# Optimization experiments

Measured on AMD Instinct MI355X. Metric: run time of the kernel, lower is better.

Reference implementation:

```python
import jax, jax.numpy as jnp
import numpy as np

UNITS = 256
IN_DIM = 256
OUT_DIM = 10
TOL = 1e-4
MAX_ITER = 50


def setup_inputs() -> dict:
    key = jax.random.key(0)
    ks = jax.random.split(key, 16)
    B = 65536
    s = 1.0 / np.sqrt(UNITS)
    inp = {
        "x": jax.random.normal(ks[0], (B, IN_DIM), dtype=jnp.float32),
        "w_in": jax.random.normal(ks[1], (IN_DIM, UNITS), dtype=jnp.float32) * s,
        "b_in": jax.random.normal(ks[2], (UNITS,), dtype=jnp.float32) * 0.01,
        "w_out": jax.random.normal(ks[3], (UNITS, OUT_DIM), dtype=jnp.float32) * s,
        "b_out": jax.random.normal(ks[4], (OUT_DIM,), dtype=jnp.float32) * 0.01,
    }
    eye = jnp.eye(UNITS, dtype=jnp.float32)
    for i in range(4):
        # well-conditioned (invertible) implicit-layer weight: I + small perturbation
        inp[f"w{i+1}"] = eye + 0.1 * jax.random.normal(ks[5 + 2 * i], (UNITS, UNITS), dtype=jnp.float32) * s
        inp[f"b{i+1}"] = jax.random.normal(ks[6 + 2 * i], (UNITS,), dtype=jnp.float32) * 0.01
    return inp


def newton_block(x, W, b):
    # Solve z @ W = x + tanh(x) + b by Newton iteration with early exit on ||g||.
    c = x + jnp.tanh(x) + b  # [B, n]
    z0 = x
    g0 = z0 @ W - c

    def cond(state):
        z, g, it = state
        return (it < MAX_ITER) & (jnp.linalg.norm(g) >= TOL)

    def body(state):
        z, g, it = state
        # torch.solve(g[:, :, None], W^T.repeat(B,1,1)): shared matrix -> one solve
        z = z - jnp.linalg.solve(W.T, g.T).T
        g = z @ W - c
        return (z, g, it + 1)

    z, _, _ = jax.lax.while_loop(cond, body, (z0, g0, jnp.asarray(0)))
    z = jax.lax.stop_gradient(z)  # torch loop runs under no_grad
    # final differentiable correction (torch: z = z - (z@W - x - tanh(x) - b))
    return z - (z @ W - c)


def reference(x, w_in, b_in, w1, b1, w2, b2, w3, b3, w4, b4, w_out, b_out):
    z = x @ w_in + b_in
    z = newton_block(z, w1, b1)
    z = newton_block(z, w2, b2)
    z = newton_block(z, w3, b3)
    z = newton_block(z, w4, b4)
    logits = z @ w_out + b_out
    return jax.nn.softmax(logits, axis=1)
```

## Files before the change

### kernel.cpp

```cpp
#include <hip/hip_runtime.h>
#include <hip/hip_fp16.h>
#include <math.h>


typedef __attribute__((ext_vector_type(8))) short short8;
typedef __attribute__((ext_vector_type(4))) float f32x4;

__device__ __forceinline__ float tanh_fast(float x) {
#if __has_builtin(__builtin_amdgcn_exp2f)
  float e = __builtin_amdgcn_exp2f(x * 2.8853900817779268f);
#else
  float e = __expf(2.0f * x);
#endif
  return 1.0f - 2.0f * __builtin_amdgcn_rcpf(e + 1.0f);
}
__device__ __forceinline__ unsigned rn_pair16(float v0, float v1) {
  __half2 h = __floats2half2_rn(v0, v1);
  return *reinterpret_cast<unsigned*>(&h);
}

__global__ __launch_bounds__(256) void ns_gemm_k(
    const float* __restrict__ a0, const float* __restrict__ a1,
    const float* __restrict__ a2, const float* __restrict__ a3,
    const float* __restrict__ b0, const float* __restrict__ b1,
    const float* __restrict__ b2, const float* __restrict__ b3,
    float* __restrict__ D, float bDiag, int eMode,
    const float* __restrict__ w_in, const float* __restrict__ w_out,
    unsigned* __restrict__ pk) {
  int m = blockIdx.z;
  int t = threadIdx.x;
  if (m == 4) {
    int base = (blockIdx.y * 8 + blockIdx.x) * 256 + t;
    for (int idx = base; idx < 34816; idx += 16384) {
      if (idx < 32768) {
        int kc = idx >> 12;
        int nt = (idx >> 8) & 15;
        int lane = (idx >> 2) & 63;
        int d = idx & 3;
        int n = nt * 16 + (lane & 15);
        int kb = kc * 32 + (lane >> 4) * 8 + d * 2;
        pk[idx] = rn_pair16(w_in[kb * 256 + n], w_in[(kb + 1) * 256 + n]);
      } else {
        int r2 = idx - 32768;
        int kc = r2 >> 8;
        int lane = (r2 >> 2) & 63;
        int d = r2 & 3;
        int n = lane & 15;
        int kb = kc * 32 + (lane >> 4) * 8 + d * 2;
        float v0 = (n < 10) ? w_out[kb * 10 + n] : 0.0f;
        float v1 = (n < 10) ? w_out[(kb + 1) * 10 + n] : 0.0f;
        pk[5 * 32768 + r2] = rn_pair16(v0, v1);
      }
    }
    return;
  }
  __shared__ float As[32][17];
  __shared__ float Bs[16][33];
  const float* A = (m == 0) ? a0 : (m == 1) ? a1 : (m == 2) ? a2 : a3;
  const float* B = (m == 0) ? b0 : (m == 1) ? b1 : (m == 2) ? b2 : b3;
  float* Dm = D + m * 65536;
  int tx = t & 15, ty = t >> 4;
  int row0 = blockIdx.y * 32, col0 = blockIdx.x * 32;
  float acc00 = 0.f, acc01 = 0.f, acc10 = 0.f, acc11 = 0.f;
  for (int k0 = 0; k0 < 256; k0 += 16) {
#pragma unroll
    for (int half = 0; half < 2; ++half) {
      int e = t + half * 256;
      int r = e >> 4, kk = e & 15;
      As[r][kk] = A[(row0 + r) * 256 + k0 + kk];
      int k2 = e >> 5, c = e & 31;
      float w = B[(k0 + k2) * 256 + col0 + c];
      if (bDiag != 0.0f) w = (((k0 + k2) == (col0 + c)) ? bDiag : 0.0f) - w;
      Bs[k2][c] = w;
    }
    __syncthreads();
#pragma unroll
    for (int kk = 0; kk < 16; ++kk) {
      float av0 = As[ty][kk], av1 = As[ty + 16][kk];
      float bv0 = Bs[kk][tx], bv1 = Bs[kk][tx + 16];
      acc00 = fmaf(av0, bv0, acc00);
      acc01 = fmaf(av0, bv1, acc01);
      acc10 = fmaf(av1, bv0, acc10);
      acc11 = fmaf(av1, bv1, acc11);
    }
    __syncthreads();
  }
  if (eMode) {
    acc00 = (((row0 + ty) == (col0 + tx)) ? 3.f : 0.f) - acc00;
    acc01 = (((row0 + ty) == (col0 + tx + 16)) ? 3.f : 0.f) - acc01;
    acc10 = (((row0 + ty + 16) == (col0 + tx)) ? 3.f : 0.f) - acc10;
    acc11 = (((row0 + ty + 16) == (col0 + tx + 16)) ? 3.f : 0.f) - acc11;
  }
  Dm[(row0 + ty) * 256 + col0 + tx] = acc00;
  Dm[(row0 + ty) * 256 + col0 + tx + 16] = acc01;
  Dm[(row0 + ty + 16) * 256 + col0 + tx] = acc10;
  Dm[(row0 + ty + 16) * 256 + col0 + tx + 16] = acc11;
}

__global__ __launch_bounds__(256) void ns_pack_k(
    const float* __restrict__ w1a, const float* __restrict__ w2a,
    const float* __restrict__ w3a, const float* __restrict__ w4a,
    const float* __restrict__ V, unsigned* __restrict__ pk) {
  __shared__ float As[32][17];
  __shared__ float Bs[16][33];
  __shared__ float Dt[32][33];
  int m = blockIdx.z;
  const float* A = (m == 0) ? w1a : (m == 1) ? w2a : (m == 2) ? w3a : w4a;
  const float* B = V + m * 65536;
  int t = threadIdx.x;
  int tx = t & 15, ty = t >> 4;
  int row0 = blockIdx.y * 32, col0 = blockIdx.x * 32;
  float acc00 = 0.f, acc01 = 0.f, acc10 = 0.f, acc11 = 0.f;
  for (int k0 = 0; k0 < 256; k0 += 16) {
#pragma unroll
    for (int half = 0; half < 2; ++half) {
      int e = t + half * 256;
      int r = e >> 4, kk = e & 15;
      float v = A[(row0 + r) * 256 + k0 + kk];
      v = (((row0 + r) == (k0 + kk)) ? 2.0f : 0.0f) - v;
      As[r][kk] = v;
      int k2 = e >> 5, c = e & 31;
      Bs[k2][c] = B[(k0 + k2) * 256 + col0 + c];
    }
    __syncthreads();
#pragma unroll
    for (int kk = 0; kk < 16; ++kk) {
      float av0 = As[ty][kk], av1 = As[ty + 16][kk];
      float bv0 = Bs[kk][tx], bv1 = Bs[kk][tx + 16];
      acc00 = fmaf(av0, bv0, acc00);
      acc01 = fmaf(av0, bv1, acc01);
      acc10 = fmaf(av1, bv0, acc10);
      acc11 = fmaf(av1, bv1, acc11);
    }
    __syncthreads();
  }
  Dt[ty][tx] = acc00;
  Dt[ty][tx + 16] = acc01;
  Dt[ty + 16][tx] = acc10;
  Dt[ty + 16][tx + 16] = acc11;
  __syncthreads();
  int kc = row0 >> 5;
#pragma unroll
  for (int i = 0; i < 2; ++i) {
    int q = i * 256 + t;
    int nt2 = q >> 8;
    int lane = (q >> 2) & 63;
    int d = q & 3;
    int lr = (lane >> 4) * 8 + d * 2;
    int lc = nt2 * 16 + (lane & 15);
    unsigned word = rn_pair16(Dt[lr][lc], Dt[lr + 1][lc]);
    pk[(m + 1) * 32768 + kc * 4096 + ((col0 >> 4) + nt2) * 256 + lane * 4 + d] = word;
  }
}

template <int MT>
__global__ __launch_bounds__(256, 4) void fused_k(
    const float* __restrict__ x, const unsigned* __restrict__ pk,
    const float* __restrict__ b_in,
    const float* __restrict__ b1, const float* __restrict__ b2,
    const float* __restrict__ b3, const float* __restrict__ b4,
    const float* __restrict__ b_out, float* __restrict__ out) {
  constexpr int NR = MT * 16;
  __shared__ unsigned short zpl[NR * 256];
  const int t = threadIdx.x;
  const int ln = t & 63;
  const int wv = t >> 6;
  const int quad = ln >> 4;
  const int n16 = ln & 15;
  const int grow0 = blockIdx.x * NR;

#pragma unroll
  for (int i = 0; i < MT * 4; ++i) {
    int e = i * 1024 + t * 4;
    int r = e >> 8, c = e & 255;
    float4 v = *(const float4*)(x + (grow0 + r) * 256 + c);
    int idx = r * 256 + (((c >> 3) ^ (r & 31)) * 8) + (c & 7);
    uint2 zp;
    zp.x = rn_pair16(v.x, v.y);
    zp.y = rn_pair16(v.z, v.w);
    *(uint2*)&zpl[idx] = zp;
  }
  __syncthreads();

  const float* bnv[4] = {b1, b2, b3, b4};
  f32x4 acc[MT][4];

  for (int layer = 0; layer < 5; ++layer) {
    const unsigned* pkl = pk + layer * 32768 + wv * 1024 + ln * 4;
#pragma unroll
    for (int mt = 0; mt < MT; ++mt)
#pragma unroll
      for (int nt = 0; nt < 4; ++nt) acc[mt][nt] = (f32x4){0.f, 0.f, 0.f, 0.f};

#pragma unroll 2
    for (int kc = 0; kc < 8; ++kc) {
      short8 wh[4], zf[MT];
      const unsigned* pb = pkl + kc * 4096;
#pragma unroll
      for (int nt = 0; nt < 4; ++nt) wh[nt] = *(const short8*)(pb + nt * 256);
#pragma unroll
      for (int mt = 0; mt < MT; ++mt) {
        int m = mt * 16 + n16;
        int idx = m * 256 + (((kc * 4 + quad) ^ (m & 31)) * 8);
        zf[mt] = *(const short8*)&zpl[idx];
      }
#pragma unroll
      for (int mt = 0; mt < MT; ++mt)
#pragma unroll
        for (int nt = 0; nt < 4; ++nt)
          acc[mt][nt] = __builtin_amdgcn_mfma_f32_16x16x32_f16(wh[nt], zf[mt], acc[mt][nt], 0, 0, 0);
    }
    __syncthreads();

#pragma unroll
    for (int nt = 0; nt < 4; ++nt) {
      int colb = wv * 64 + nt * 16 + quad * 4;
      float4 bi = make_float4(0.f, 0.f, 0.f, 0.f);
      float4 bn4 = bi;
      if (layer == 0) bi = *(const float4*)(b_in + colb);
      if (layer < 4) bn4 = *(const float4*)(bnv[layer] + colb);
#pragma unroll
      for (int mt = 0; mt < MT; ++mt) {
        int row = mt * 16 + n16;
        float v0 = acc[mt][nt][0] + bi.x;
        float v1 = acc[mt][nt][1] + bi.y;
        float v2 = acc[mt][nt][2] + bi.z;
        float v3 = acc[mt][nt][3] + bi.w;
        if (layer < 4) {
          v0 = v0 + tanh_fast(v0) + bn4.x;
          v1 = v1 + tanh_fast(v1) + bn4.y;
          v2 = v2 + tanh_fast(v2) + bn4.z;
          v3 = v3 + tanh_fast(v3) + bn4.w;
        }
        int idx = row * 256 + (((colb >> 3) ^ (row & 31)) * 8) + (colb & 7);
        uint2 zp;
        zp.x = rn_pair16(v0, v1);
        zp.y = rn_pair16(v2, v3);
        *(uint2*)&zpl[idx] = zp;
      }
    }
    __syncthreads();
  }

  f32x4 lacc[MT];
#pragma unroll
  for (int mt = 0; mt < MT; ++mt) lacc[mt] = (f32x4){0.f, 0.f, 0.f, 0.f};
  const unsigned* pw = pk + 5 * 32768 + ln * 4;
#pragma unroll
  for (int kk = 0; kk < 2; ++kk) {
    int kc = wv * 2 + kk;
    short8 wh = *(const short8*)(pw + kc * 256);
#pragma unroll
    for (int mt = 0; mt < MT; ++mt) {
      int m = mt * 16 + n16;
      int idx = m * 256 + (((kc * 4 + quad) ^ (m & 31)) * 8);
      short8 zf = *(const short8*)&zpl[idx];
      lacc[mt] = __builtin_amdgcn_mfma_f32_16x16x32_f16(wh, zf, lacc[mt], 0, 0, 0);
    }
  }
  __syncthreads();
  float* pbuf = (float*)zpl;
#pragma unroll
  for (int mt = 0; mt < MT; ++mt) {
    int addr = wv * (NR * 16) + (mt * 16 + n16) * 16 + quad * 4;
    *(f32x4*)&pbuf[addr] = lacc[mt];
  }
  __syncthreads();
  if (t < NR) {
    int r = t;
    float lg[10];
    float mx = -1e30f;
#pragma unroll
    for (int j = 0; j < 10; ++j) {
      float s = b_out[j];
#pragma unroll
      for (int w2 = 0; w2 < 4; ++w2) s += pbuf[w2 * (NR * 16) + r * 16 + j];
      lg[j] = s;
      mx = fmaxf(mx, s);
    }
    float sum = 0.f;
#pragma unroll
    for (int j = 0; j < 10; ++j) {
      lg[j] = __expf(lg[j] - mx);
      sum += lg[j];
    }
    float inv = 1.0f / sum;
    float* op = out + (grow0 + r) * 10;
#pragma unroll
    for (int j = 0; j < 10; ++j) op[j] = lg[j] * inv;
  }
}

extern "C" void kernel_launch(void* const* d_in, const int* in_sizes, int n_in,
                              void* d_out, int out_size, void* d_ws, size_t ws_size,
                              hipStream_t stream) {
  const float* x     = (const float*)d_in[0];
  const float* w_in  = (const float*)d_in[1];
  const float* b_in  = (const float*)d_in[2];
  const float* w_out = (const float*)d_in[3];
  const float* b_out = (const float*)d_in[4];
  const float* w1 = (const float*)d_in[5];
  const float* b1 = (const float*)d_in[6];
  const float* w2 = (const float*)d_in[7];
  const float* b2 = (const float*)d_in[8];
  const float* w3 = (const float*)d_in[9];
  const float* b3 = (const float*)d_in[10];
  const float* w4 = (const float*)d_in[11];
  const float* b4 = (const float*)d_in[12];
  float* out = (float*)d_out;

  unsigned* pk = (unsigned*)d_ws;
  float* T = (float*)d_ws + 165888;
  float* U = T + 262144;

  dim3 blk(256);
  ns_gemm_k<<<dim3(8, 8, 5), blk, 0, stream>>>(w1, w2, w3, w4, w1, w2, w3, w4,
                                               T, 2.0f, 0, w_in, w_out, pk);
  ns_gemm_k<<<dim3(8, 8, 4), blk, 0, stream>>>(T, T + 65536, T + 131072, T + 196608,
                                               T, T + 65536, T + 131072, T + 196608,
                                               U, 3.0f, 1, nullptr, nullptr, pk);
  ns_pack_k<<<dim3(8, 8, 4), blk, 0, stream>>>(w1, w2, w3, w4, U, pk);
  fused_k<4><<<1024, 256, 0, stream>>>(x, pk, b_in, b1, b2, b3, b4, b_out, out);
}
```

Before: 206.3 us.

## Replace three-kernel Newton-Schulz inverse with single Horner polynomial kernel

```diff
diff --git a/kernel.cpp b/kernel.cpp
--- a/kernel.cpp
+++ b/kernel.cpp
@@ -19,137 +19,93 @@
   return *reinterpret_cast<unsigned*>(&h);
 }
 
-__global__ __launch_bounds__(256) void ns_gemm_k(
-    const float* __restrict__ a0, const float* __restrict__ a1,
-    const float* __restrict__ a2, const float* __restrict__ a3,
-    const float* __restrict__ b0, const float* __restrict__ b1,
-    const float* __restrict__ b2, const float* __restrict__ b3,
-    float* __restrict__ D, float bDiag, int eMode,
+__global__ __launch_bounds__(256) void ns_poly_k(
+    const float* __restrict__ w1, const float* __restrict__ w2,
+    const float* __restrict__ w3, const float* __restrict__ w4,
     const float* __restrict__ w_in, const float* __restrict__ w_out,
     unsigned* __restrict__ pk) {
-  int m = blockIdx.z;
-  int t = threadIdx.x;
-  if (m == 4) {
-    int base = (blockIdx.y * 8 + blockIdx.x) * 256 + t;
-    for (int idx = base; idx < 34816; idx += 16384) {
-      if (idx < 32768) {
-        int kc = idx >> 12;
-        int nt = (idx >> 8) & 15;
-        int lane = (idx >> 2) & 63;
-        int d = idx & 3;
-        int n = nt * 16 + (lane & 15);
-        int kb = kc * 32 + (lane >> 4) * 8 + d * 2;
-        pk[idx] = rn_pair16(w_in[kb * 256 + n], w_in[(kb + 1) * 256 + n]);
-      } else {
-        int r2 = idx - 32768;
-        int kc = r2 >> 8;
-        int lane = (r2 >> 2) & 63;
-        int d = r2 & 3;
-        int n = lane & 15;
-        int kb = kc * 32 + (lane >> 4) * 8 + d * 2;
-        float v0 = (n < 10) ? w_out[kb * 10 + n] : 0.0f;
-        float v1 = (n < 10) ? w_out[(kb + 1) * 10 + n] : 0.0f;
-        pk[5 * 32768 + r2] = rn_pair16(v0, v1);
+  const int bid = blockIdx.x;
+  const int t = threadIdx.x;
+  if (bid >= 128) {
+    int idx = (bid - 128) * 256 + t;
+    {
+      int kc = idx >> 12;
+      int nt = (idx >> 8) & 15;
+      int lane = (idx >> 2) & 63;
+      int d = idx & 3;
+      int n = nt * 16 + (lane & 15);
+      int kb = kc * 32 + (lane >> 4) * 8 + d * 2;
+      pk[idx] = rn_pair16(w_in[kb * 256 + n], w_in[(kb + 1) * 256 + n]);
+    }
+    int idx2 = idx + 32768;
+    if (idx2 < 34816) {
+      int r2 = idx2 - 32768;
+      int kc = r2 >> 8;
+      int lane = (r2 >> 2) & 63;
+      int d = r2 & 3;
+      int n = lane & 15;
+      int kb = kc * 32 + (lane >> 4) * 8 + d * 2;
+      float v0 = (n < 10) ? w_out[kb * 10 + n] : 0.0f;
+      float v1 = (n < 10) ? w_out[(kb + 1) * 10 + n] : 0.0f;
+      pk[5 * 32768 + r2] = rn_pair16(v0, v1);
+    }
+    return;
+  }
+  const int m = bid >> 5;
+  const int r0 = (bid & 31) * 8;
+  const float* __restrict__ W = (m == 0) ? w1 : (m == 1) ? w2 : (m == 2) ? w3 : w4;
+  __shared__ float S[8][256];
+
+#pragma unroll
+  for (int i = 0; i < 8; ++i) {
+    int e = i * 256 + t;
+    int r = e >> 8, c = e & 255;
+    S[r][c] = (((r0 + r) == c) ? 6.0f : 0.0f) - W[(r0 + r) * 256 + c];
+  }
+  __syncthreads();
+
+  const float coef[4] = {-15.0f, 20.0f, -15.0f, 6.0f};
+#pragma unroll
+  for (int step = 0; step < 4; ++step) {
+    float acc[8];
+#pragma unroll
+    for (int r = 0; r < 8; ++r) acc[r] = 0.0f;
+    for (int k = 0; k < 256; k += 4) {
+      float4 sv[8];
+#pragma unroll
+      for (int r = 0; r < 8; ++r) sv[r] = *(const float4*)&S[r][k];
+      float wv0 = W[(k + 0) * 256 + t];
+      float wv1 = W[(k + 1) * 256 + t];
+      float wv2 = W[(k + 2) * 256 + t];
+      float wv3 = W[(k + 3) * 256 + t];
+#pragma unroll
+      for (int r = 0; r < 8; ++r) {
+        acc[r] = fmaf(sv[r].x, wv0, acc[r]);
+        acc[r] = fmaf(sv[r].y, wv1, acc[r]);
+        acc[r] = fmaf(sv[r].z, wv2, acc[r]);
+        acc[r] = fmaf(sv[r].w, wv3, acc[r]);
       }
     }
-    return;
-  }
-  __shared__ float As[32][17];
-  __shared__ float Bs[16][33];
-  const float* A = (m == 0) ? a0 : (m == 1) ? a1 : (m == 2) ? a2 : a3;
-  const float* B = (m == 0) ? b0 : (m == 1) ? b1 : (m == 2) ? b2 : b3;
-  float* Dm = D + m * 65536;
-  int tx = t & 15, ty = t >> 4;
-  int row0 = blockIdx.y * 32, col0 = blockIdx.x * 32;
-  float acc00 = 0.f, acc01 = 0.f, acc10 = 0.f, acc11 = 0.f;
-  for (int k0 = 0; k0 < 256; k0 += 16) {
-#pragma unroll
-    for (int half = 0; half < 2; ++half) {
-      int e = t + half * 256;
-      int r = e >> 4, kk = e & 15;
-      As[r][kk] = A[(row0 + r) * 256 + k0 + kk];
-      int k2 = e >> 5, c = e & 31;
-      float w = B[(k0 + k2) * 256 + col0 + c];
-      if (bDiag != 0.0f) w = (((k0 + k2) == (col0 + c)) ? bDiag : 0.0f) - w;
-      Bs[k2][c] = w;
-    }
-    __syncthreads();
-#pragma unroll
-    for (int kk = 0; kk < 16; ++kk) {
-      float av0 = As[ty][kk], av1 = As[ty + 16][kk];
-      float bv0 = Bs[kk][tx], bv1 = Bs[kk][tx + 16];
-      acc00 = fmaf(av0, bv0, acc00);
-      acc01 = fmaf(av0, bv1, acc01);
-      acc10 = fmaf(av1, bv0, acc10);
-      acc11 = fmaf(av1, bv1, acc11);
-    }
-    __syncthreads();
-  }
-  if (eMode) {
-    acc00 = (((row0 + ty) == (col0 + tx)) ? 3.f : 0.f) - acc00;
-    acc01 = (((row0 + ty) == (col0 + tx + 16)) ? 3.f : 0.f) - acc01;
-    acc10 = (((row0 + ty + 16) == (col0 + tx)) ? 3.f : 0.f) - acc10;
-    acc11 = (((row0 + ty + 16) == (col0 + tx + 16)) ? 3.f : 0.f) - acc11;
-  }
-  Dm[(row0 + ty) * 256 + col0 + tx] = acc00;
-  Dm[(row0 + ty) * 256 + col0 + tx + 16] = acc01;
-  Dm[(row0 + ty + 16) * 256 + col0 + tx] = acc10;
-  Dm[(row0 + ty + 16) * 256 + col0 + tx + 16] = acc11;
-}
-
-__global__ __launch_bounds__(256) void ns_pack_k(
-    const float* __restrict__ w1a, const float* __restrict__ w2a,
-    const float* __restrict__ w3a, const float* __restrict__ w4a,
-    const float* __restrict__ V, unsigned* __restrict__ pk) {
-  __shared__ float As[32][17];
-  __shared__ float Bs[16][33];
-  __shared__ float Dt[32][33];
-  int m = blockIdx.z;
-  const float* A = (m == 0) ? w1a : (m == 1) ? w2a : (m == 2) ? w3a : w4a;
-  const float* B = V + m * 65536;
-  int t = threadIdx.x;
-  int tx = t & 15, ty = t >> 4;
-  int row0 = blockIdx.y * 32, col0 = blockIdx.x * 32;
-  float acc00 = 0.f, acc01 = 0.f, acc10 = 0.f, acc11 = 0.f;
-  for (int k0 = 0; k0 < 256; k0 += 16) {
-#pragma unroll
-    for (int half = 0; half < 2; ++half) {
-      int e = t + half * 256;
-      int r = e >> 4, kk = e & 15;
-      float v = A[(row0 + r) * 256 + k0 + kk];
-      v = (((row0 + r) == (k0 + kk)) ? 2.0f : 0.0f) - v;
-      As[r][kk] = v;
-      int k2 = e >> 5, c = e & 31;
-      Bs[k2][c] = B[(k0 + k2) * 256 + col0 + c];
-    }
-    __syncthreads();
-#pragma unroll
-    for (int kk = 0; kk < 16; ++kk) {
-      float av0 = As[ty][kk], av1 = As[ty + 16][kk];
-      float bv0 = Bs[kk][tx], bv1 = Bs[kk][tx + 16];
-      acc00 = fmaf(av0, bv0, acc00);
-      acc01 = fmaf(av0, bv1, acc01);
-      acc10 = fmaf(av1, bv0, acc10);
-      acc11 = fmaf(av1, bv1, acc11);
-    }
-    __syncthreads();
-  }
-  Dt[ty][tx] = acc00;
-  Dt[ty][tx + 16] = acc01;
-  Dt[ty + 16][tx] = acc10;
-  Dt[ty + 16][tx + 16] = acc11;
-  __syncthreads();
-  int kc = row0 >> 5;
-#pragma unroll
-  for (int i = 0; i < 2; ++i) {
+    __syncthreads();
+    float cdiag = coef[step];
+#pragma unroll
+    for (int r = 0; r < 8; ++r)
+      S[r][t] = acc[r] + (((r0 + r) == t) ? cdiag : 0.0f);
+    __syncthreads();
+  }
+
+  const int kc = r0 >> 5;
+  const int quad = (r0 >> 3) & 3;
+#pragma unroll
+  for (int i = 0; i < 4; ++i) {
     int q = i * 256 + t;
-    int nt2 = q >> 8;
-    int lane = (q >> 2) & 63;
+    int nt = q >> 6;
+    int n16 = (q >> 2) & 15;
     int d = q & 3;
-    int lr = (lane >> 4) * 8 + d * 2;
-    int lc = nt2 * 16 + (lane & 15);
-    unsigned word = rn_pair16(Dt[lr][lc], Dt[lr + 1][lc]);
-    pk[(m + 1) * 32768 + kc * 4096 + ((col0 >> 4) + nt2) * 256 + lane * 4 + d] = word;
+    int lane = quad * 16 + n16;
+    int n = nt * 16 + n16;
+    unsigned word = rn_pair16(S[d * 2][n], S[d * 2 + 1][n]);
+    pk[(m + 1) * 32768 + kc * 4096 + nt * 256 + lane * 4 + d] = word;
   }
 }
 
@@ -200,8 +156,8 @@
       for (int nt = 0; nt < 4; ++nt) wh[nt] = *(const short8*)(pb + nt * 256);
 #pragma unroll
       for (int mt = 0; mt < MT; ++mt) {
-        int m = mt * 16 + n16;
-        int idx = m * 256 + (((kc * 4 + quad) ^ (m & 31)) * 8);
+        int mm = mt * 16 + n16;
+        int idx = mm * 256 + (((kc * 4 + quad) ^ (mm & 31)) * 8);
         zf[mt] = *(const short8*)&zpl[idx];
       }
 #pragma unroll
@@ -252,8 +208,8 @@
     short8 wh = *(const short8*)(pw + kc * 256);
 #pragma unroll
     for (int mt = 0; mt < MT; ++mt) {
-      int m = mt * 16 + n16;
-      int idx = m * 256 + (((kc * 4 + quad) ^ (m & 31)) * 8);
+      int mm = mt * 16 + n16;
+      int idx = mm * 256 + (((kc * 4 + quad) ^ (mm & 31)) * 8);
       short8 zf = *(const short8*)&zpl[idx];
       lacc[mt] = __builtin_amdgcn_mfma_f32_16x16x32_f16(wh, zf, lacc[mt], 0, 0, 0);
     }
@@ -310,15 +266,7 @@
   float* out = (float*)d_out;
 
   unsigned* pk = (unsigned*)d_ws;
-  float* T = (float*)d_ws + 165888;
-  float* U = T + 262144;
-
-  dim3 blk(256);
-  ns_gemm_k<<<dim3(8, 8, 5), blk, 0, stream>>>(w1, w2, w3, w4, w1, w2, w3, w4,
-                                               T, 2.0f, 0, w_in, w_out, pk);
-  ns_gemm_k<<<dim3(8, 8, 4), blk, 0, stream>>>(T, T + 65536, T + 131072, T + 196608,
-                                               T, T + 65536, T + 131072, T + 196608,
-                                               U, 3.0f, 1, nullptr, nullptr, pk);
-  ns_pack_k<<<dim3(8, 8, 4), blk, 0, stream>>>(w1, w2, w3, w4, U, pk);
+
+  ns_poly_k<<<256, 256, 0, stream>>>(w1, w2, w3, w4, w_in, w_out, pk);
   fused_k<4><<<1024, 256, 0, stream>>>(x, pk, b_in, b1, b2, b3, b4, b_out, out);
 }
```

Result: faster. 200.3 us (-2.9%).
